# Performance work log

Hardware: AMD Instinct MI355X
Metric: run time of the kernel (lower is better)

Reference implementation:

```python
import jax, jax.numpy as jnp
import numpy as np

EPS = 1e-5
H = 6  # num_heads

def batchnorm(x, g, b):
    # BatchNorm1d over node dim using batch statistics (biased var, eps=1e-5)
    mu = x.mean(0)
    var = jnp.mean((x - mu) ** 2, 0)
    return (x - mu) * jax.lax.rsqrt(var + EPS) * g + b

def setup_inputs() -> dict:
    key = jax.random.key(0)
    ks = jax.random.split(key, 16)
    N, E, D = 20000, 200000, 384
    DH = 2 * D  # mlp hidden = dim * mlp_ratio(2.0)
    s = 0.05
    lin = lambda k, i, o: jax.random.normal(k, (i, o), jnp.float32) * s
    inp = {}
    inp['x'] = jax.random.normal(ks[0], (N, D), jnp.float32)
    inp['edge_index'] = jax.random.randint(ks[1], (2, E), 0, N)
    inp['edge_attr'] = jax.random.normal(ks[2], (E, D), jnp.float32)
    # norm1
    inp['g1'] = jnp.ones((D,), jnp.float32); inp['b1'] = jnp.zeros((D,), jnp.float32)
    # TransformerConv-style attention (concat=True, beta=False, edge_dim=D)
    inp['Wq'] = lin(ks[3], D, D); inp['bq'] = jnp.zeros((D,), jnp.float32)
    inp['Wk'] = lin(ks[4], D, D); inp['bk'] = jnp.zeros((D,), jnp.float32)
    inp['Wv'] = lin(ks[5], D, D); inp['bv'] = jnp.zeros((D,), jnp.float32)
    inp['We'] = lin(ks[6], D, D)  # lin_edge, no bias
    inp['Wskip'] = lin(ks[7], D, D); inp['bskip'] = jnp.zeros((D,), jnp.float32)
    # norm2
    inp['g2'] = jnp.ones((D,), jnp.float32); inp['b2'] = jnp.zeros((D,), jnp.float32)
    # Mlp
    inp['W1'] = lin(ks[8], D, DH); inp['bm1'] = jnp.zeros((DH,), jnp.float32)
    inp['W2'] = lin(ks[9], DH, D); inp['bm2'] = jnp.zeros((D,), jnp.float32)
    return inp

def reference(x, edge_index, edge_attr, g1, b1, Wq, bq, Wk, bk, Wv, bv, We, Wskip, bskip, g2, b2, W1, bm1, W2, bm2):
    N, D = x.shape
    Dh = D // H
    scale = 1.0 / jnp.sqrt(jnp.float32(Dh))
    h = batchnorm(x, g1, b1)
    q = (h @ Wq + bq).reshape(N, H, Dh)
    k = (h @ Wk + bk).reshape(N, H, Dh)
    v = (h @ Wv + bv).reshape(N, H, Dh)
    e = (edge_attr @ We).reshape(-1, H, Dh)  # [E,H,Dh]
    src, dst = edge_index[0], edge_index[1]
    ke = k[src] + e  # edge attr added to key
    ve = v[src] + e  # and to value (PyG TransformerConv)
    logits = jnp.einsum('ehd,ehd->eh', q[dst], ke) * scale  # [E,H]
    # segment softmax over incoming edges of each dst node
    m = jax.ops.segment_max(logits, dst, num_segments=N)
    a = jnp.exp(logits - m[dst])
    ssum = jax.ops.segment_sum(a, dst, num_segments=N)
    denom = ssum[dst]
    a = a / jnp.where(denom == 0, 1.0, denom)
    agg = jax.ops.segment_sum(a[:, :, None] * ve, dst, num_segments=N).reshape(N, D)
    attn = agg + (h @ Wskip + bskip)  # root skip (lin_skip)
    x = x + attn  # residual 1 (drop_path/dropout disabled in eval)
    h2 = batchnorm(x, g2, b2)
    mlp = jax.nn.gelu(h2 @ W1 + bm1, approximate=False) @ W2 + bm2
    return x + mlp
```

## Files before the change

### kernel.cpp

```cpp
#include <hip/hip_runtime.h>
#include <hip/hip_bf16.h>

#define DD 384
#define NH 6
#define DHID 768

typedef __attribute__((ext_vector_type(8))) short bf16x8;
typedef __attribute__((ext_vector_type(4))) float f32x4;

__device__ __forceinline__ void gload_lds16(const void* gsrc, void* ldst) {
  __builtin_amdgcn_global_load_lds((const __attribute__((address_space(1))) void*)gsrc,
                                   (__attribute__((address_space(3))) void*)ldst,
                                   16, 0, 0);
}

__device__ __forceinline__ float b2f(unsigned short u) {
  union { unsigned int i; float f; } c;
  c.i = (unsigned int)u << 16;
  return c.f;
}

__device__ __forceinline__ short f2bf(float x) {
  union { __hip_bfloat16 h; short s; } u;
  u.h = __float2bfloat16(x);
  return u.s;
}

__global__ __launch_bounds__(384) void bn_stats_k(const float* __restrict__ x, float* __restrict__ sums,
                                                  float* __restrict__ sq, int N, int rpb) {
  int d = threadIdx.x;
  int r0 = blockIdx.x * rpb;
  int r1 = min(r0 + rpb, N);
  float s = 0.f, ss = 0.f;
  for (int r = r0; r < r1; ++r) {
    float v = x[(size_t)r * DD + d];
    s += v; ss += v * v;
  }
  atomicAdd(&sums[d], s);
  atomicAdd(&sq[d], ss);
}

__global__ void bn_finalize_k(const float* sums, const float* sq, const float* g, const float* b,
                              float* a, float* c, int N) {
  int d = blockIdx.x * blockDim.x + threadIdx.x;
  if (d >= DD) return;
  float inv = 1.f / (float)N;
  float mu = sums[d] * inv;
  float var = sq[d] * inv - mu * mu;
  float rs = rsqrtf(var + 1e-5f);
  a[d] = rs * g[d];
  c[d] = b[d] - mu * rs * g[d];
}

union BPack { ushort4 u; __hip_bfloat16 b[4]; };

__global__ void norm_to_bf16_k(const float* __restrict__ x, const float* __restrict__ a,
                               const float* __restrict__ c, __hip_bfloat16* __restrict__ h, int total4) {
  int i = blockIdx.x * blockDim.x + threadIdx.x;
  if (i >= total4) return;
  float4 v = ((const float4*)x)[i];
  int d0 = (i * 4) % DD;
  float4 av = *(const float4*)(a + d0);
  float4 cv = *(const float4*)(c + d0);
  BPack p;
  p.b[0] = __float2bfloat16(v.x * av.x + cv.x);
  p.b[1] = __float2bfloat16(v.y * av.y + cv.y);
  p.b[2] = __float2bfloat16(v.z * av.z + cv.z);
  p.b[3] = __float2bfloat16(v.w * av.w + cv.w);
  ((ushort4*)h)[i] = p.u;
}

__global__ void transpose_bf16_k(const float* __restrict__ in, __hip_bfloat16* __restrict__ out,
                                 int K, int Nout) {
  int i = blockIdx.x * blockDim.x + threadIdx.x;
  if (i >= K * Nout) return;
  int k = i / Nout, n = i % Nout;
  out[(size_t)n * K + k] = __float2bfloat16(in[i]);
}

__global__ void concat_bias_k(const float* bq, const float* bk, const float* bv, const float* bs,
                              float* out) {
  int i = blockIdx.x * blockDim.x + threadIdx.x;
  if (i >= 1536) return;
  float v = (i < 384) ? bq[i] : (i < 768) ? bk[i - 384] : (i < 1152) ? bv[i - 768] : bs[i - 1152];
  out[i] = v;
}

__global__ void add3_k(const float* __restrict__ x, const float* __restrict__ agg,
                       const float* __restrict__ skip, float* __restrict__ x1, int total4) {
  int i = blockIdx.x * blockDim.x + threadIdx.x;
  if (i >= total4) return;
  float4 a = ((const float4*)x)[i];
  float4 b = ((const float4*)agg)[i];
  float4 c = ((const float4*)skip)[i];
  float4 o;
  o.x = a.x + b.x + c.x; o.y = a.y + b.y + c.y;
  o.z = a.z + b.z + c.z; o.w = a.w + b.w + c.w;
  ((float4*)x1)[i] = o;
}

__global__ void hist_k(const int* __restrict__ ei, int* __restrict__ deg, int E) {
  int i = blockIdx.x * blockDim.x + threadIdx.x;
  if (i < E) atomicAdd(&deg[ei[E + i]], 1);
}

__global__ __launch_bounds__(1024) void scan_k(const int* __restrict__ deg, int* __restrict__ row_start,
                                               int* __restrict__ cursor, int N) {
  __shared__ int part[1024];
  int t = threadIdx.x;
  int ch = (N + 1023) / 1024;
  int c0 = t * ch, c1 = min(c0 + ch, N);
  int s = 0;
  for (int i = c0; i < c1; ++i) s += deg[i];
  part[t] = s;
  __syncthreads();
  for (int off = 1; off < 1024; off <<= 1) {
    int v = (t >= off) ? part[t - off] : 0;
    __syncthreads();
    part[t] += v;
    __syncthreads();
  }
  int run = part[t] - s;
  for (int i = c0; i < c1; ++i) {
    row_start[i] = run; cursor[i] = run; run += deg[i];
  }
  if (t == 1023) row_start[N] = part[1023];
}

__global__ void scatter_k(const int* __restrict__ ei, int* __restrict__ cursor,
                          int* __restrict__ csr_src, int* __restrict__ csr_eid, int E) {
  int i = blockIdx.x * blockDim.x + threadIdx.x;
  if (i >= E) return;
  int s = ei[i], d = ei[E + i];
  int pos = atomicAdd(&cursor[d], 1);
  csr_src[pos] = s;
  csr_eid[pos] = i;
}

__global__ __launch_bounds__(256) void attn_k(const __hip_bfloat16* __restrict__ qkv,
                                              const __hip_bfloat16* __restrict__ ebuf,
                                              const int* __restrict__ row_start,
                                              const int* __restrict__ csr_src,
                                              const int* __restrict__ csr_eid,
                                              float* __restrict__ agg, int N) {
  int wid = (blockIdx.x * blockDim.x + threadIdx.x) >> 6;
  int lane = threadIdx.x & 63;
  if (wid >= N) return;
  int g = lane >> 4, l = lane & 15;
  const ushort* qk = (const ushort*)qkv;
  const ushort* eu = (const ushort*)ebuf;
  float q[NH][4], acc[NH][4], psum[NH];
#pragma unroll
  for (int h = 0; h < NH; ++h) {
    ushort4 u = *(const ushort4*)&qk[(size_t)wid * 1152 + h * 64 + l * 4];
    q[h][0] = b2f(u.x); q[h][1] = b2f(u.y); q[h][2] = b2f(u.z); q[h][3] = b2f(u.w);
#pragma unroll
    for (int j = 0; j < 4; ++j) acc[h][j] = 0.f;
    psum[h] = 0.f;
  }
  int i0 = row_start[wid], i1 = row_start[wid + 1];
  for (int i = i0; i < i1; i += 4) {
    int e = i + g;
    bool valid = e < i1;
    int ec = valid ? e : i1 - 1;
    size_t sb = (size_t)csr_src[ec] * 1152;
    size_t eb = (size_t)csr_eid[ec] * 384;
    float ev[NH][4], p[NH];
#pragma unroll
    for (int h = 0; h < NH; ++h) {
      ushort4 ue = *(const ushort4*)&eu[eb + h * 64 + l * 4];
      ev[h][0] = b2f(ue.x); ev[h][1] = b2f(ue.y); ev[h][2] = b2f(ue.z); ev[h][3] = b2f(ue.w);
      ushort4 uk = *(const ushort4*)&qk[sb + 384 + h * 64 + l * 4];
      float t = q[h][0] * (b2f(uk.x) + ev[h][0]);
      t += q[h][1] * (b2f(uk.y) + ev[h][1]);
      t += q[h][2] * (b2f(uk.z) + ev[h][2]);
      t += q[h][3] * (b2f(uk.w) + ev[h][3]);
      t += __shfl_xor(t, 1);
      t += __shfl_xor(t, 2);
      t += __shfl_xor(t, 4);
      t += __shfl_xor(t, 8);
      p[h] = valid ? __expf(t * 0.125f) : 0.f;
    }
#pragma unroll
    for (int h = 0; h < NH; ++h) {
      ushort4 uv = *(const ushort4*)&qk[sb + 768 + h * 64 + l * 4];
      acc[h][0] += p[h] * (b2f(uv.x) + ev[h][0]);
      acc[h][1] += p[h] * (b2f(uv.y) + ev[h][1]);
      acc[h][2] += p[h] * (b2f(uv.z) + ev[h][2]);
      acc[h][3] += p[h] * (b2f(uv.w) + ev[h][3]);
      psum[h] += p[h];
    }
  }
#pragma unroll
  for (int h = 0; h < NH; ++h) {
#pragma unroll
    for (int j = 0; j < 4; ++j) {
      acc[h][j] += __shfl_xor(acc[h][j], 16);
      acc[h][j] += __shfl_xor(acc[h][j], 32);
    }
    psum[h] += __shfl_xor(psum[h], 16);
    psum[h] += __shfl_xor(psum[h], 32);
  }
  if (lane < 16) {
#pragma unroll
    for (int h = 0; h < NH; ++h) {
      float inv = psum[h] > 0.f ? 1.f / psum[h] : 0.f;
      float4 o;
      o.x = acc[h][0] * inv; o.y = acc[h][1] * inv;
      o.z = acc[h][2] * inv; o.w = acc[h][3] * inv;
      *(float4*)&agg[(size_t)wid * DD + h * 64 + l * 4] = o;
    }
  }
}

#define BM 128
#define BN 128
#define BK 32

enum { M_QKVS = 0, M_BF16 = 1, M_GELU = 2, M_RES = 3 };

template <int MODE, int AF32>
__global__ __launch_bounds__(256) void gemm_k(const void* __restrict__ Aab,
                                              const __hip_bfloat16* __restrict__ BT,
                                              const float* __restrict__ bias,
                                              const float* __restrict__ res,
                                              void* __restrict__ out0, void* __restrict__ out1,
                                              int M, int K, int Nn) {
  __shared__ short lA[BM * BK];
  __shared__ short lB[BN * BK];
  int t = threadIdx.x;
  int lane = t & 63, w = t >> 6;
  int wr = (w >> 1) * 64, wc = (w & 1) * 64;
  int row0 = blockIdx.y * BM, col0 = blockIdx.x * BN;
  int lr = lane & 15, lk = lane >> 4;
  f32x4 acc[4][4] = {};

  for (int kt = 0; kt < K; kt += BK) {
    __syncthreads();
#pragma unroll
    for (int j = 0; j < 2; ++j) {
      int chunk = j * 256 + t;
      int r = chunk >> 2, kc = chunk & 3;
      int wavebase = (j * 256 + w * 64) * 8;
      gload_lds16(BT + (size_t)(col0 + r) * K + kt + kc * 8, &lB[wavebase]);
    }
    if constexpr (AF32) {
      const float* Af = (const float*)Aab;
#pragma unroll
      for (int pass = 0; pass < 2; ++pass) {
        int c = pass * 256 + t;
        int r = c >> 2, kc = c & 3;
        int gra = row0 + r; gra = gra < M ? gra : M - 1;
        const float4* ap = (const float4*)(Af + (size_t)gra * K + kt + kc * 8);
        float4 f0 = ap[0], f1 = ap[1];
        bf16x8 v;
        v[0] = f2bf(f0.x); v[1] = f2bf(f0.y); v[2] = f2bf(f0.z); v[3] = f2bf(f0.w);
        v[4] = f2bf(f1.x); v[5] = f2bf(f1.y); v[6] = f2bf(f1.z); v[7] = f2bf(f1.w);
        *(__shared__ bf16x8*)&lA[c * 8] = v;
      }
    } else {
      const __hip_bfloat16* A = (const __hip_bfloat16*)Aab;
#pragma unroll
      for (int j = 0; j < 2; ++j) {
        int chunk = j * 256 + t;
        int r = chunk >> 2, kc = chunk & 3;
        int wavebase = (j * 256 + w * 64) * 8;
        int gra = row0 + r; gra = gra < M ? gra : M - 1;
        gload_lds16(A + (size_t)gra * K + kt + kc * 8, &lA[wavebase]);
      }
    }
    __syncthreads();
    bf16x8 af[4], bfr[4];
#pragma unroll
    for (int mi = 0; mi < 4; ++mi)
      af[mi] = *(const bf16x8*)&lA[(wr + mi * 16 + lr) * BK + lk * 8];
#pragma unroll
    for (int ni = 0; ni < 4; ++ni)
      bfr[ni] = *(const bf16x8*)&lB[(wc + ni * 16 + lr) * BK + lk * 8];
#pragma unroll
    for (int mi = 0; mi < 4; ++mi)
#pragma unroll
      for (int ni = 0; ni < 4; ++ni)
        acc[mi][ni] = __builtin_amdgcn_mfma_f32_16x16x32_bf16(af[mi], bfr[ni], acc[mi][ni], 0, 0, 0);
  }

#pragma unroll
  for (int mi = 0; mi < 4; ++mi) {
#pragma unroll
    for (int r = 0; r < 4; ++r) {
      int row = row0 + wr + mi * 16 + lk * 4 + r;
      if (row >= M) continue;
#pragma unroll
      for (int ni = 0; ni < 4; ++ni) {
        int col = col0 + wc + ni * 16 + lr;
        float v = acc[mi][ni][r];
        if constexpr (MODE == M_QKVS) {
          v += bias[col];
          if (col < 1152)
            ((__hip_bfloat16*)out0)[(size_t)row * 1152 + col] = __float2bfloat16(v);
          else
            ((float*)out1)[(size_t)row * DD + (col - 1152)] = v;
        } else if constexpr (MODE == M_BF16) {
          ((__hip_bfloat16*)out0)[(size_t)row * Nn + col] = __float2bfloat16(v);
        } else if constexpr (MODE == M_GELU) {
          v += bias[col];
          v = 0.5f * v * (1.f + erff(v * 0.70710678118f));
          ((__hip_bfloat16*)out0)[(size_t)row * Nn + col] = __float2bfloat16(v);
        } else {
          v += bias[col];
          ((float*)out0)[(size_t)row * Nn + col] = v + res[(size_t)row * Nn + col];
        }
      }
    }
  }
}

extern "C" void kernel_launch(void* const* d_in, const int* in_sizes, int n_in,
                              void* d_out, int out_size, void* d_ws, size_t ws_size,
                              hipStream_t stream) {
  const float* x   = (const float*)d_in[0];
  const int*   ei  = (const int*)d_in[1];
  const float* ea  = (const float*)d_in[2];
  const float* g1  = (const float*)d_in[3];
  const float* b1  = (const float*)d_in[4];
  const float* Wq  = (const float*)d_in[5];
  const float* bq  = (const float*)d_in[6];
  const float* Wk  = (const float*)d_in[7];
  const float* bk  = (const float*)d_in[8];
  const float* Wv  = (const float*)d_in[9];
  const float* bv  = (const float*)d_in[10];
  const float* We  = (const float*)d_in[11];
  const float* Wsk = (const float*)d_in[12];
  const float* bsk = (const float*)d_in[13];
  const float* g2  = (const float*)d_in[14];
  const float* b2  = (const float*)d_in[15];
  const float* W1  = (const float*)d_in[16];
  const float* bm1 = (const float*)d_in[17];
  const float* W2  = (const float*)d_in[18];
  const float* bm2 = (const float*)d_in[19];

  int N = in_sizes[0] / DD;
  int E = in_sizes[1] / 2;

  char* ws = (char*)d_ws;
  size_t off = 0;
  auto alloc = [&](size_t bytes) -> char* {
    char* p = ws + off;
    off = (off + bytes + 255) & ~(size_t)255;
    return p;
  };

  float* bnsum = (float*)alloc(4 * DD * sizeof(float));
  float* a1 = (float*)alloc(DD * 4);
  float* c1 = (float*)alloc(DD * 4);
  float* a2 = (float*)alloc(DD * 4);
  float* c2 = (float*)alloc(DD * 4);
  float* bqkvs = (float*)alloc(1536 * 4);
  __hip_bfloat16* WqkvsT = (__hip_bfloat16*)alloc((size_t)1536 * DD * 2);
  __hip_bfloat16* WeT = (__hip_bfloat16*)alloc((size_t)DD * DD * 2);
  __hip_bfloat16* W1T = (__hip_bfloat16*)alloc((size_t)DHID * DD * 2);
  __hip_bfloat16* W2T = (__hip_bfloat16*)alloc((size_t)DD * DHID * 2);
  __hip_bfloat16* hbuf = (__hip_bfloat16*)alloc((size_t)N * DD * 2);
  __hip_bfloat16* qkv = (__hip_bfloat16*)alloc((size_t)N * 1152 * 2);
  float* skip = (float*)alloc((size_t)N * DD * 4);
  __hip_bfloat16* ebuf = (__hip_bfloat16*)alloc((size_t)E * DD * 2);
  float* agg = (float*)alloc((size_t)N * DD * 4);
  float* x1 = (float*)alloc((size_t)N * DD * 4);
  __hip_bfloat16* hid = (__hip_bfloat16*)alloc((size_t)N * DHID * 2);
  int* deg = (int*)alloc((size_t)N * 4);
  int* cursor = (int*)alloc((size_t)N * 4);
  int* row_start = (int*)alloc((size_t)(N + 1) * 4);
  int* csr_src = (int*)alloc((size_t)E * 4);
  int* csr_eid = (int*)alloc((size_t)E * 4);
  (void)ws_size; (void)n_in; (void)out_size;

  hipMemsetAsync(bnsum, 0, 4 * DD * sizeof(float), stream);
  hipMemsetAsync(deg, 0, (size_t)N * 4, stream);

  int rpb = 128, sgrid = (N + rpb - 1) / rpb;
  bn_stats_k<<<sgrid, DD, 0, stream>>>(x, bnsum, bnsum + DD, N, rpb);
  bn_finalize_k<<<2, 256, 0, stream>>>(bnsum, bnsum + DD, g1, b1, a1, c1, N);

  int t4 = N * DD / 4;
  norm_to_bf16_k<<<(t4 + 255) / 256, 256, 0, stream>>>(x, a1, c1, hbuf, t4);

  int wgrid = (DD * DD + 255) / 256;
  transpose_bf16_k<<<wgrid, 256, 0, stream>>>(Wq, WqkvsT, DD, DD);
  transpose_bf16_k<<<wgrid, 256, 0, stream>>>(Wk, WqkvsT + (size_t)DD * DD, DD, DD);
  transpose_bf16_k<<<wgrid, 256, 0, stream>>>(Wv, WqkvsT + (size_t)2 * DD * DD, DD, DD);
  transpose_bf16_k<<<wgrid, 256, 0, stream>>>(Wsk, WqkvsT + (size_t)3 * DD * DD, DD, DD);
  transpose_bf16_k<<<wgrid, 256, 0, stream>>>(We, WeT, DD, DD);
  transpose_bf16_k<<<(DD * DHID + 255) / 256, 256, 0, stream>>>(W1, W1T, DD, DHID);
  transpose_bf16_k<<<(DHID * DD + 255) / 256, 256, 0, stream>>>(W2, W2T, DHID, DD);
  concat_bias_k<<<6, 256, 0, stream>>>(bq, bk, bv, bsk, bqkvs);

  dim3 gqkvs(1536 / BN, (N + BM - 1) / BM);
  gemm_k<M_QKVS, 0><<<gqkvs, 256, 0, stream>>>(hbuf, WqkvsT, bqkvs, nullptr, qkv, skip, N, DD, 1536);

  dim3 ge(DD / BN, (E + BM - 1) / BM);
  gemm_k<M_BF16, 1><<<ge, 256, 0, stream>>>(ea, WeT, nullptr, nullptr, ebuf, nullptr, E, DD, DD);

  hist_k<<<(E + 255) / 256, 256, 0, stream>>>(ei, deg, E);
  scan_k<<<1, 1024, 0, stream>>>(deg, row_start, cursor, N);
  scatter_k<<<(E + 255) / 256, 256, 0, stream>>>(ei, cursor, csr_src, csr_eid, E);

  attn_k<<<(N * 64 + 255) / 256, 256, 0, stream>>>(qkv, ebuf, row_start, csr_src, csr_eid, agg, N);

  add3_k<<<(t4 + 255) / 256, 256, 0, stream>>>(x, agg, skip, x1, t4);

  bn_stats_k<<<sgrid, DD, 0, stream>>>(x1, bnsum + 2 * DD, bnsum + 3 * DD, N, rpb);
  bn_finalize_k<<<2, 256, 0, stream>>>(bnsum + 2 * DD, bnsum + 3 * DD, g2, b2, a2, c2, N);
  norm_to_bf16_k<<<(t4 + 255) / 256, 256, 0, stream>>>(x1, a2, c2, hbuf, t4);

  dim3 gm1(DHID / BN, (N + BM - 1) / BM);
  gemm_k<M_GELU, 0><<<gm1, 256, 0, stream>>>(hbuf, W1T, bm1, nullptr, hid, nullptr, N, DD, DHID);

  dim3 gm2(DD / BN, (N + BM - 1) / BM);
  gemm_k<M_RES, 0><<<gm2, 256, 0, stream>>>(hid, W2T, bm2, x1, (float*)d_out, nullptr, N, DHID, DD);
}
```

Measured before the change: 630.7 us.

## Use full-width N tile for edge GEMM to read fp32 edge_attr once

Adds a dedicated edge-projection GEMM whose block covers all 384 output columns, so each row tile of the fp32 edge_attr is loaded and converted to bf16 only once instead of once per column tile. Each wave holds a 64x192 accumulator tile (48 MFMA accumulators), which raises register pressure and may lower occupancy. The B tile in LDS grows to 384xBK.

```diff
diff --git a/kernel.cpp b/kernel.cpp
--- a/kernel.cpp
+++ b/kernel.cpp
@@ -310,6 +310,68 @@
           v += bias[col];
           ((float*)out0)[(size_t)row * Nn + col] = v + res[(size_t)row * Nn + col];
         }
+      }
+    }
+  }
+}
+
+__global__ __launch_bounds__(256, 2) void gemm_edge_wide(const float* __restrict__ A,
+                                                         const __hip_bfloat16* __restrict__ BT,
+                                                         __hip_bfloat16* __restrict__ out, int M) {
+  __shared__ short lA[BM * BK];
+  __shared__ short lB[DD * BK];
+  int t = threadIdx.x;
+  int lane = t & 63, w = t >> 6;
+  int wr = (w >> 1) * 64, wc = (w & 1) * 192;
+  int row0 = blockIdx.x * BM;
+  int lr = lane & 15, lk = lane >> 4;
+  f32x4 acc[4][12] = {};
+
+  for (int kt = 0; kt < DD; kt += BK) {
+    __syncthreads();
+#pragma unroll
+    for (int p = 0; p < 6; ++p) {
+      int c = p * 256 + t;
+      int r = c >> 2, kc = c & 3;
+      int wavebase = (p * 256 + w * 64) * 8;
+      gload_lds16(BT + (size_t)r * DD + kt + kc * 8, &lB[wavebase]);
+    }
+#pragma unroll
+    for (int pass = 0; pass < 2; ++pass) {
+      int c = pass * 256 + t;
+      int r = c >> 2, kc = c & 3;
+      int gra = row0 + r; gra = gra < M ? gra : M - 1;
+      const float4* ap = (const float4*)(A + (size_t)gra * DD + kt + kc * 8);
+      float4 f0 = ap[0], f1 = ap[1];
+      bf16x8 v;
+      v[0] = f2bf(f0.x); v[1] = f2bf(f0.y); v[2] = f2bf(f0.z); v[3] = f2bf(f0.w);
+      v[4] = f2bf(f1.x); v[5] = f2bf(f1.y); v[6] = f2bf(f1.z); v[7] = f2bf(f1.w);
+      *(__shared__ bf16x8*)&lA[c * 8] = v;
+    }
+    __syncthreads();
+    bf16x8 af[4];
+#pragma unroll
+    for (int mi = 0; mi < 4; ++mi)
+      af[mi] = *(const bf16x8*)&lA[(wr + mi * 16 + lr) * BK + lk * 8];
+#pragma unroll
+    for (int ni = 0; ni < 12; ++ni) {
+      bf16x8 bfr = *(const bf16x8*)&lB[(wc + ni * 16 + lr) * BK + lk * 8];
+#pragma unroll
+      for (int mi = 0; mi < 4; ++mi)
+        acc[mi][ni] = __builtin_amdgcn_mfma_f32_16x16x32_bf16(af[mi], bfr, acc[mi][ni], 0, 0, 0);
+    }
+  }
+
+#pragma unroll
+  for (int mi = 0; mi < 4; ++mi) {
+#pragma unroll
+    for (int r = 0; r < 4; ++r) {
+      int row = row0 + wr + mi * 16 + lk * 4 + r;
+      if (row >= M) continue;
+#pragma unroll
+      for (int ni = 0; ni < 12; ++ni) {
+        int col = wc + ni * 16 + lr;
+        out[(size_t)row * DD + col] = __float2bfloat16(acc[mi][ni][r]);
       }
     }
   }
@@ -397,8 +459,7 @@
   dim3 gqkvs(1536 / BN, (N + BM - 1) / BM);
   gemm_k<M_QKVS, 0><<<gqkvs, 256, 0, stream>>>(hbuf, WqkvsT, bqkvs, nullptr, qkv, skip, N, DD, 1536);
 
-  dim3 ge(DD / BN, (E + BM - 1) / BM);
-  gemm_k<M_BF16, 1><<<ge, 256, 0, stream>>>(ea, WeT, nullptr, nullptr, ebuf, nullptr, E, DD, DD);
+  gemm_edge_wide<<<(E + BM - 1) / BM, 256, 0, stream>>>(ea, WeT, ebuf, E);
 
   hist_k<<<(E + 255) / 256, 256, 0, stream>>>(ei, deg, E);
   scan_k<<<1, 1024, 0, stream>>>(deg, row_start, cursor, N);
```

Measured after the change: 595.8 us. 1.06x faster.
